# Kernel tuning notes

Hardware: AMD Instinct MI355X
Metric: run time of the kernel (lower is better)

## Reference

```python
import jax, jax.numpy as jnp
import numpy as np

B, S, H, DH = 2, 4096, 8, 64
D = H * DH


def setup_inputs() -> dict:
    key = jax.random.key(0)
    ks = jax.random.split(key, 6)
    std = 1.0 / np.sqrt(D)
    return {
        "x": jax.random.normal(ks[0], (B, S, D), dtype=jnp.float32),
        "Wq": jax.random.normal(ks[1], (D, D), dtype=jnp.float32) * std,
        "Wk": jax.random.normal(ks[2], (D, D), dtype=jnp.float32) * std,
        "Wv": jax.random.normal(ks[3], (D, D), dtype=jnp.float32) * std,
        "Wo": jax.random.normal(ks[4], (D, D), dtype=jnp.float32) * std,
        "bo": jnp.zeros((D,), dtype=jnp.float32),
    }


def reference(x, Wq, Wk, Wv, Wo, bo):
    scale = DH ** (-0.5)
    # torch Linear: y = x @ W.T
    q = x @ Wq.T  # [B,S,D]
    k = x @ Wk.T
    v = x @ Wv.T
    # split heads -> [B,H,S,Dh]
    q = q.reshape(B, S, H, DH).transpose(0, 2, 1, 3)
    k = k.reshape(B, S, H, DH).transpose(0, 2, 1, 3)
    v = v.reshape(B, S, H, DH).transpose(0, 2, 1, 3)
    score = jnp.einsum('bhqd,bhkd->bhqk', q, k) * scale  # [B,H,S,S]
    weights = jax.nn.softmax(score, axis=-1)
    attn = jnp.einsum('bhqk,bhkd->bhqd', weights, v)  # [B,H,S,Dh]
    h_ = attn.transpose(0, 2, 1, 3).reshape(B, S, D)
    return h_ @ Wo.T + bo
```

## Files before the change

### kernel.cpp

```cpp
#include <hip/hip_runtime.h>

#define LOG2E 1.44269504088896340736f

typedef unsigned short u16;
typedef __bf16 bf16x4_t __attribute__((ext_vector_type(4)));
typedef __bf16 bf16x8_t __attribute__((ext_vector_type(8)));
typedef float f32x4_t __attribute__((ext_vector_type(4)));

__device__ __forceinline__ f32x4_t mfma16(bf16x8_t a, bf16x8_t b, f32x4_t c) {
  return __builtin_amdgcn_mfma_f32_16x16x32_bf16(a, b, c, 0, 0, 0);
}

__device__ __forceinline__ void gl_lds16(const u16* g, u16* l) {
  __builtin_amdgcn_global_load_lds(
      (const __attribute__((address_space(1))) unsigned int*)g,
      (__attribute__((address_space(3))) unsigned int*)l, 16, 0, 0);
}

__global__ __launch_bounds__(256) void cast_kernel(
    const float* __restrict__ x, const float* __restrict__ Wq, const float* __restrict__ Wk,
    const float* __restrict__ Wv, const float* __restrict__ Wo,
    u16* __restrict__ Xb, u16* __restrict__ Wqb, u16* __restrict__ Wkb,
    u16* __restrict__ Wvb, u16* __restrict__ Wob) {
  const int bid = blockIdx.x;
  const float* src;
  u16* dst;
  float scale = 1.f;
  int rel;
  if (bid < 2048)      { src = x;  dst = Xb;  rel = bid; }
  else if (bid < 2176) { src = Wq; dst = Wqb; rel = bid - 2048; scale = 0.125f * LOG2E; }
  else if (bid < 2304) { src = Wk; dst = Wkb; rel = bid - 2176; }
  else if (bid < 2432) { src = Wv; dst = Wvb; rel = bid - 2304; }
  else                 { src = Wo; dst = Wob; rel = bid - 2432; }
  const int i = rel * 2048 + threadIdx.x * 8;
  f32x4_t a = *(const f32x4_t*)(src + i) * scale;
  f32x4_t b = *(const f32x4_t*)(src + i + 4) * scale;
  union { uint4 u; struct { bf16x4_t lo, hi; } s; } c;
  c.s.lo = __builtin_convertvector(a, bf16x4_t);
  c.s.hi = __builtin_convertvector(b, bf16x4_t);
  *(uint4*)(dst + i) = c.u;
}

template <int MODE>
__device__ __forceinline__ void gemm_core_bf16(const u16* __restrict__ A, const u16* __restrict__ Bt,
                                               void* __restrict__ Cout, const float* __restrict__ bo,
                                               int Mbase, int Nbase) {
  __shared__ __align__(16) u16 As[128][64];
  __shared__ __align__(16) u16 Bs[128][64];
  const int t = threadIdx.x;
  const int wave = t >> 6, lane = t & 63;
  const int r = lane & 15, qd = lane >> 4;
  const int wm = wave & 1, wn = wave >> 1;
  const int rr = lane >> 3;
  const int s8 = ((lane & 7) ^ (rr & 7)) * 8;

  f32x4_t acc[4][4];
#pragma unroll
  for (int i = 0; i < 4; i++)
#pragma unroll
    for (int j = 0; j < 4; j++) { f32x4_t z = {0.f, 0.f, 0.f, 0.f}; acc[i][j] = z; }

  const u16* pa = A  + (Mbase + wave * 32 + rr) * 512 + s8;
  const u16* pb = Bt + (Nbase + wave * 32 + rr) * 512 + s8;
  u16* la = &As[wave * 32][0];
  u16* lb = &Bs[wave * 32][0];

  for (int k0 = 0; k0 < 512; k0 += 64) {
#pragma unroll
    for (int j = 0; j < 4; j++) gl_lds16(pa + k0 + j * 8 * 512, la + j * 8 * 64);
#pragma unroll
    for (int j = 0; j < 4; j++) gl_lds16(pb + k0 + j * 8 * 512, lb + j * 8 * 64);
    __syncthreads();
#pragma unroll
    for (int h = 0; h < 2; h++) {
      bf16x8_t af[4], bfr[4];
#pragma unroll
      for (int i = 0; i < 4; i++)
        af[i]  = *(const bf16x8_t*)&As[wm * 64 + i * 16 + r][((h * 4 + qd) ^ (r & 7)) * 8];
#pragma unroll
      for (int j = 0; j < 4; j++)
        bfr[j] = *(const bf16x8_t*)&Bs[wn * 64 + j * 16 + r][((h * 4 + qd) ^ (r & 7)) * 8];
#pragma unroll
      for (int i = 0; i < 4; i++)
#pragma unroll
        for (int j = 0; j < 4; j++) acc[i][j] = mfma16(af[i], bfr[j], acc[i][j]);
    }
    __syncthreads();
  }

  float bv[4];
  if (MODE == 2) {
#pragma unroll
    for (int j = 0; j < 4; j++) bv[j] = bo[Nbase + wn * 64 + j * 16 + r];
  }
#pragma unroll
  for (int i = 0; i < 4; i++) {
#pragma unroll
    for (int reg = 0; reg < 4; reg++) {
      int gr = Mbase + wm * 64 + i * 16 + qd * 4 + reg;
#pragma unroll
      for (int j = 0; j < 4; j++) {
        int gc = Nbase + wn * 64 + j * 16 + r;
        float val = acc[i][j][reg];
        if (MODE == 1) {
          int bb = gc >> 12, ss = gc & 4095;
          ((__bf16*)Cout)[((long)(bb * 512 + gr)) * 4096 + ss] = (__bf16)val;
        } else if (MODE == 0) {
          ((__bf16*)Cout)[gr * 512 + gc] = (__bf16)val;
        } else {
          ((float*)Cout)[gr * 512 + gc] = val + bv[j];
        }
      }
    }
  }
}

__global__ __launch_bounds__(256) void gemm_qkv_kernel(
    const u16* __restrict__ Xb,
    const u16* __restrict__ Wqb, const u16* __restrict__ Wkb, const u16* __restrict__ Wvb,
    u16* __restrict__ Q, u16* __restrict__ K, u16* __restrict__ Vt) {
  if (blockIdx.z == 0)
    gemm_core_bf16<0>(Xb, Wqb, Q, nullptr, blockIdx.x * 128, blockIdx.y * 128);
  else if (blockIdx.z == 1)
    gemm_core_bf16<0>(Xb, Wkb, K, nullptr, blockIdx.x * 128, blockIdx.y * 128);
  else
    gemm_core_bf16<1>(Wvb, Xb, Vt, nullptr, blockIdx.y * 128, blockIdx.x * 128);
}

__global__ __launch_bounds__(256) void gemm_out_kernel(
    const u16* __restrict__ Aat, const u16* __restrict__ Wob,
    float* __restrict__ Out, const float* __restrict__ bo) {
  gemm_core_bf16<2>(Aat, Wob, Out, bo, blockIdx.x * 128, blockIdx.y * 128);
}

__global__ __launch_bounds__(256, 2) void attn_kernel(
    const u16* __restrict__ Q, const u16* __restrict__ K, const u16* __restrict__ Vt,
    u16* __restrict__ Oattn) {
  __shared__ __align__(16) u16 Ks[2][2][4096];
  __shared__ __align__(16) u16 Vs[2][2][4096];

  const int t = threadIdx.x;
  const int wave = t >> 6, lane = t & 63;
  const int r = lane & 15, qd = lane >> 4;
  const int g = wave & 1, kv = wave >> 1;
  const int bh = blockIdx.y;
  const int b = bh >> 3, h = bh & 7;
  const long bbase = (long)b * 4096 * 512;
  const int q0 = blockIdx.x * 128;

  const int sw = r & 7;
  const int ck0 = (qd ^ sw) * 8;
  const int ck1 = ((qd + 4) ^ sw) * 8;
  int vo0[2], vo1[2];
#pragma unroll
  for (int c = 0; c < 2; c++) {
    vo0[c] = ((c * 4 + (qd >> 1)) ^ sw) * 8 + 4 * (qd & 1);
    vo1[c] = ((c * 4 + 2 + (qd >> 1)) ^ sw) * 8 + 4 * (qd & 1);
  }

  bf16x8_t ones8;
#pragma unroll
  for (int j = 0; j < 8; j++) ones8[j] = (__bf16)1.0f;

  bf16x8_t qf[4][2];
#pragma unroll
  for (int qa = 0; qa < 4; qa++) {
    const u16* qp = Q + bbase + (long)(q0 + g * 64 + qa * 16 + r) * 512 + h * 64 + qd * 8;
    qf[qa][0] = *(const bf16x8_t*)(qp);
    qf[qa][1] = *(const bf16x8_t*)(qp + 32);
  }

  f32x4_t accO[4][4];
  f32x4_t accL[4];
#pragma unroll
  for (int qa = 0; qa < 4; qa++) {
    f32x4_t z = {0.f, 0.f, 0.f, 0.f};
    accL[qa] = z;
#pragma unroll
    for (int nt = 0; nt < 4; nt++) accO[qa][nt] = z;
  }

  const int rr = lane >> 3;
  const int cc = (lane & 7) ^ rr;
  const u16* kgb = K + bbase + (long)(kv * 2048 + g * 32 + rr) * 512 + h * 64 + cc * 8;
  const u16* vgb = Vt + ((long)(b * 512 + h * 64 + g * 32 + rr)) * 4096 + kv * 2048 + cc * 8;

#pragma unroll
  for (int i = 0; i < 4; i++) gl_lds16(kgb + (long)i * 8 * 512, &Ks[kv][0][g * 2048] + i * 512);
#pragma unroll
  for (int i = 0; i < 4; i++) gl_lds16(vgb + i * 8 * 4096, &Vs[kv][0][g * 2048] + i * 512);

  for (int it = 0; it < 32; it++) {
    const int buf = it & 1;
    __syncthreads();

    if (it < 31) {
      const int nb = (it + 1) & 1;
      const long ko = (long)(it + 1) * 64;
#pragma unroll
      for (int i = 0; i < 4; i++)
        gl_lds16(kgb + (ko + i * 8) * 512, &Ks[kv][nb][g * 2048] + i * 512);
#pragma unroll
      for (int i = 0; i < 4; i++)
        gl_lds16(vgb + ko + (long)i * 8 * 4096, &Vs[kv][nb][g * 2048] + i * 512);
    }

    bf16x8_t kf[4][2];
#pragma unroll
    for (int nt = 0; nt < 4; nt++) {
      const u16* kb = &Ks[kv][buf][(nt * 16 + r) * 64];
      kf[nt][0] = *(const bf16x8_t*)(kb + ck0);
      kf[nt][1] = *(const bf16x8_t*)(kb + ck1);
    }

    f32x4_t St[4][4];
    __builtin_amdgcn_s_setprio(1);
#pragma unroll
    for (int qa = 0; qa < 4; qa++)
#pragma unroll
      for (int nt = 0; nt < 4; nt++) {
        f32x4_t z = {0.f, 0.f, 0.f, 0.f};
        z = mfma16(kf[nt][0], qf[qa][0], z);
        z = mfma16(kf[nt][1], qf[qa][1], z);
        St[qa][nt] = z;
      }
    __builtin_amdgcn_s_setprio(0);

    bf16x8_t pf[4][2];
#pragma unroll
    for (int qa = 0; qa < 4; qa++)
#pragma unroll
      for (int c = 0; c < 2; c++) {
        f32x4_t e0, e1;
#pragma unroll
        for (int j = 0; j < 4; j++) {
          e0[j] = __builtin_amdgcn_exp2f(St[qa][2 * c][j]);
          e1[j] = __builtin_amdgcn_exp2f(St[qa][2 * c + 1][j]);
        }
        bf16x4_t b0 = __builtin_convertvector(e0, bf16x4_t);
        bf16x4_t b1 = __builtin_convertvector(e1, bf16x4_t);
        bf16x8_t p8;
#pragma unroll
        for (int j = 0; j < 4; j++) { p8[j] = b0[j]; p8[4 + j] = b1[j]; }
        pf[qa][c] = p8;
      }

#pragma unroll
    for (int qa = 0; qa < 4; qa++)
#pragma unroll
      for (int c = 0; c < 2; c++)
        accL[qa] = mfma16(ones8, pf[qa][c], accL[qa]);

#pragma unroll
    for (int c = 0; c < 2; c++) {
      bf16x8_t va[4];
#pragma unroll
      for (int dm = 0; dm < 4; dm++) {
        const u16* vb = &Vs[kv][buf][(dm * 16 + r) * 64];
        union { uint4 u; bf16x8_t v; } cat;
        *(uint2*)&cat.u.x = *(const uint2*)(vb + vo0[c]);
        *(uint2*)&cat.u.z = *(const uint2*)(vb + vo1[c]);
        va[dm] = cat.v;
      }
      __builtin_amdgcn_s_setprio(1);
#pragma unroll
      for (int qa = 0; qa < 4; qa++)
#pragma unroll
        for (int dm = 0; dm < 4; dm++)
          accO[qa][dm] = mfma16(va[dm], pf[qa][c], accO[qa][dm]);
      __builtin_amdgcn_s_setprio(0);
    }
  }

  __syncthreads();
  float* Sc  = (float*)&Ks[0][0][0];
  float* Lsc = (float*)&Vs[0][0][0];
  if (kv == 1) {
#pragma unroll
    for (int qa = 0; qa < 4; qa++) {
#pragma unroll
      for (int dm = 0; dm < 4; dm++)
        *(f32x4_t*)&Sc[g * 4096 + ((qa * 4 + dm) * 64 + lane) * 4] = accO[qa][dm];
      Lsc[g * 256 + qa * 64 + lane] = accL[qa][0];
    }
  }
  __syncthreads();
  if (kv == 0) {
#pragma unroll
    for (int qa = 0; qa < 4; qa++) {
      float L = accL[qa][0] + Lsc[g * 256 + qa * 64 + lane];
      float inv = 1.f / L;
      int gq = q0 + g * 64 + qa * 16 + r;
#pragma unroll
      for (int dm = 0; dm < 4; dm++) {
        f32x4_t o = *(const f32x4_t*)&Sc[g * 4096 + ((qa * 4 + dm) * 64 + lane) * 4];
        o += accO[qa][dm];
        bf16x4_t ob;
#pragma unroll
        for (int reg = 0; reg < 4; reg++) ob[reg] = (__bf16)(o[reg] * inv);
        *(uint2*)&Oattn[bbase + (long)gq * 512 + h * 64 + dm * 16 + qd * 4] = *(uint2*)&ob;
      }
    }
  }
}

extern "C" void kernel_launch(void* const* d_in, const int* in_sizes, int n_in,
                              void* d_out, int out_size, void* d_ws, size_t ws_size,
                              hipStream_t stream) {
  const float* x  = (const float*)d_in[0];
  const float* Wq = (const float*)d_in[1];
  const float* Wk = (const float*)d_in[2];
  const float* Wv = (const float*)d_in[3];
  const float* Wo = (const float*)d_in[4];
  const float* bo = (const float*)d_in[5];
  float* out = (float*)d_out;

  u16* ws  = (u16*)d_ws;
  u16* Qb  = ws;
  u16* Kb  = Qb  + 4194304;
  u16* Vtg = Kb  + 4194304;
  u16* Ab  = Vtg + 4194304;
  u16* Xb  = Ab;
  u16* Wqb = Ab  + 4194304;
  u16* Wkb = Wqb + 262144;
  u16* Wvb = Wkb + 262144;
  u16* Wob = Wvb + 262144;

  cast_kernel<<<2560, 256, 0, stream>>>(x, Wq, Wk, Wv, Wo, Xb, Wqb, Wkb, Wvb, Wob);

  dim3 g1(64, 4, 3);
  gemm_qkv_kernel<<<g1, 256, 0, stream>>>(Xb, Wqb, Wkb, Wvb, Qb, Kb, Vtg);

  dim3 g2(32, 16);
  attn_kernel<<<g2, 256, 0, stream>>>(Qb, Kb, Vtg, Ab);

  dim3 g3(64, 4);
  gemm_out_kernel<<<g3, 256, 0, stream>>>(Ab, Wob, out, bo);
}
```

Baseline: 186.7 us.

## Fuse QKV projections into one kernel with shared X tile and LDS-staged stores

```diff
diff --git a/kernel.cpp b/kernel.cpp
--- a/kernel.cpp
+++ b/kernel.cpp
@@ -41,96 +41,171 @@
   *(uint4*)(dst + i) = c.u;
 }
 
-template <int MODE>
-__device__ __forceinline__ void gemm_core_bf16(const u16* __restrict__ A, const u16* __restrict__ Bt,
-                                               void* __restrict__ Cout, const float* __restrict__ bo,
-                                               int Mbase, int Nbase) {
-  __shared__ __align__(16) u16 As[128][64];
-  __shared__ __align__(16) u16 Bs[128][64];
+__global__ __launch_bounds__(512) void gemm_qkv_fused(
+    const u16* __restrict__ Xb,
+    const u16* __restrict__ Wqb, const u16* __restrict__ Wkb, const u16* __restrict__ Wvb,
+    u16* __restrict__ Q, u16* __restrict__ K, u16* __restrict__ Vt) {
+  __shared__ __align__(16) u16 SM[28672];
+  u16 (*As)[64] = (u16(*)[64])SM;
+  u16 (*Bq)[64] = (u16(*)[64])(SM + 4096);
+  u16 (*Bk)[64] = (u16(*)[64])(SM + 12288);
+  u16 (*Bv)[64] = (u16(*)[64])(SM + 20480);
   const int t = threadIdx.x;
   const int wave = t >> 6, lane = t & 63;
   const int r = lane & 15, qd = lane >> 4;
-  const int wm = wave & 1, wn = wave >> 1;
+  const int wn = wave;
   const int rr = lane >> 3;
   const int s8 = ((lane & 7) ^ (rr & 7)) * 8;
-
-  f32x4_t acc[4][4];
+  const int Mbase = blockIdx.x * 64, Nbase = blockIdx.y * 128;
+
+  f32x4_t acc[3][4];
+#pragma unroll
+  for (int w = 0; w < 3; w++)
+#pragma unroll
+    for (int i = 0; i < 4; i++) { f32x4_t z = {0.f, 0.f, 0.f, 0.f}; acc[w][i] = z; }
+
+  const u16* pa = Xb  + (Mbase + wave * 8 + rr) * 512 + s8;
+  const u16* pq = Wqb + (Nbase + wave * 16 + rr) * 512 + s8;
+  const u16* pk = Wkb + (Nbase + wave * 16 + rr) * 512 + s8;
+  const u16* pv = Wvb + (Nbase + wave * 16 + rr) * 512 + s8;
+  u16* la = &As[wave * 8][0];
+  u16* lq = &Bq[wave * 16][0];
+  u16* lk = &Bk[wave * 16][0];
+  u16* lv = &Bv[wave * 16][0];
+
+  for (int k0 = 0; k0 < 512; k0 += 64) {
+    gl_lds16(pa + k0, la);
+#pragma unroll
+    for (int p = 0; p < 2; p++) {
+      gl_lds16(pq + k0 + p * 8 * 512, lq + p * 512);
+      gl_lds16(pk + k0 + p * 8 * 512, lk + p * 512);
+      gl_lds16(pv + k0 + p * 8 * 512, lv + p * 512);
+    }
+    __syncthreads();
+#pragma unroll
+    for (int h = 0; h < 2; h++) {
+      const int cs = ((h * 4 + qd) ^ (r & 7)) * 8;
+      bf16x8_t af[4];
+#pragma unroll
+      for (int i = 0; i < 4; i++) af[i] = *(const bf16x8_t*)&As[i * 16 + r][cs];
+      bf16x8_t fq = *(const bf16x8_t*)&Bq[wn * 16 + r][cs];
+      bf16x8_t fk = *(const bf16x8_t*)&Bk[wn * 16 + r][cs];
+      bf16x8_t fv = *(const bf16x8_t*)&Bv[wn * 16 + r][cs];
+#pragma unroll
+      for (int i = 0; i < 4; i++) {
+        acc[0][i] = mfma16(af[i], fq, acc[0][i]);
+        acc[1][i] = mfma16(af[i], fk, acc[1][i]);
+        acc[2][i] = mfma16(af[i], fv, acc[2][i]);
+      }
+    }
+    __syncthreads();
+  }
+
+#pragma unroll
+  for (int w = 0; w < 2; w++) {
+    __syncthreads();
+    u16* dst = (w == 0) ? Q : K;
+#pragma unroll
+    for (int i = 0; i < 4; i++)
+#pragma unroll
+      for (int reg = 0; reg < 4; reg++) {
+        int row = i * 16 + qd * 4 + reg;
+        int col = wn * 16 + r;
+        __bf16 bvv = (__bf16)acc[w][i][reg];
+        SM[row * 128 + (col ^ (((row >> 2) & 7) << 3))] = *(u16*)&bvv;
+      }
+    __syncthreads();
+#pragma unroll
+    for (int p = 0; p < 2; p++) {
+      int row = p * 32 + (t >> 4);
+      int col = (t & 15) * 8;
+      uint4 v = *(const uint4*)&SM[row * 128 + (col ^ (((row >> 2) & 7) << 3))];
+      *(uint4*)&dst[(Mbase + row) * 512 + Nbase + col] = v;
+    }
+  }
+  __syncthreads();
 #pragma unroll
   for (int i = 0; i < 4; i++)
 #pragma unroll
-    for (int j = 0; j < 4; j++) { f32x4_t z = {0.f, 0.f, 0.f, 0.f}; acc[i][j] = z; }
-
-  const u16* pa = A  + (Mbase + wave * 32 + rr) * 512 + s8;
-  const u16* pb = Bt + (Nbase + wave * 32 + rr) * 512 + s8;
-  u16* la = &As[wave * 32][0];
-  u16* lb = &Bs[wave * 32][0];
-
-  for (int k0 = 0; k0 < 512; k0 += 64) {
-#pragma unroll
-    for (int j = 0; j < 4; j++) gl_lds16(pa + k0 + j * 8 * 512, la + j * 8 * 64);
-#pragma unroll
-    for (int j = 0; j < 4; j++) gl_lds16(pb + k0 + j * 8 * 512, lb + j * 8 * 64);
-    __syncthreads();
-#pragma unroll
-    for (int h = 0; h < 2; h++) {
-      bf16x8_t af[4], bfr[4];
-#pragma unroll
-      for (int i = 0; i < 4; i++)
-        af[i]  = *(const bf16x8_t*)&As[wm * 64 + i * 16 + r][((h * 4 + qd) ^ (r & 7)) * 8];
-#pragma unroll
-      for (int j = 0; j < 4; j++)
-        bfr[j] = *(const bf16x8_t*)&Bs[wn * 64 + j * 16 + r][((h * 4 + qd) ^ (r & 7)) * 8];
-#pragma unroll
-      for (int i = 0; i < 4; i++)
-#pragma unroll
-        for (int j = 0; j < 4; j++) acc[i][j] = mfma16(af[i], bfr[j], acc[i][j]);
-    }
-    __syncthreads();
-  }
-
-  float bv[4];
-  if (MODE == 2) {
-#pragma unroll
-    for (int j = 0; j < 4; j++) bv[j] = bo[Nbase + wn * 64 + j * 16 + r];
-  }
-#pragma unroll
-  for (int i = 0; i < 4; i++) {
-#pragma unroll
     for (int reg = 0; reg < 4; reg++) {
-      int gr = Mbase + wm * 64 + i * 16 + qd * 4 + reg;
-#pragma unroll
-      for (int j = 0; j < 4; j++) {
-        int gc = Nbase + wn * 64 + j * 16 + r;
-        float val = acc[i][j][reg];
-        if (MODE == 1) {
-          int bb = gc >> 12, ss = gc & 4095;
-          ((__bf16*)Cout)[((long)(bb * 512 + gr)) * 4096 + ss] = (__bf16)val;
-        } else if (MODE == 0) {
-          ((__bf16*)Cout)[gr * 512 + gc] = (__bf16)val;
-        } else {
-          ((float*)Cout)[gr * 512 + gc] = val + bv[j];
-        }
-      }
-    }
-  }
-}
-
-__global__ __launch_bounds__(256) void gemm_qkv_kernel(
-    const u16* __restrict__ Xb,
-    const u16* __restrict__ Wqb, const u16* __restrict__ Wkb, const u16* __restrict__ Wvb,
-    u16* __restrict__ Q, u16* __restrict__ K, u16* __restrict__ Vt) {
-  if (blockIdx.z == 0)
-    gemm_core_bf16<0>(Xb, Wqb, Q, nullptr, blockIdx.x * 128, blockIdx.y * 128);
-  else if (blockIdx.z == 1)
-    gemm_core_bf16<0>(Xb, Wkb, K, nullptr, blockIdx.x * 128, blockIdx.y * 128);
-  else
-    gemm_core_bf16<1>(Wvb, Xb, Vt, nullptr, blockIdx.y * 128, blockIdx.x * 128);
-}
-
-__global__ __launch_bounds__(256) void gemm_out_kernel(
+      int srow = i * 16 + qd * 4 + reg;
+      int dcol = wn * 16 + r;
+      __bf16 bvv = (__bf16)acc[2][i][reg];
+      SM[dcol * 64 + (srow ^ (((dcol >> 2) & 7) << 3))] = *(u16*)&bvv;
+    }
+  __syncthreads();
+  {
+    const int bb = Mbase >> 12;
+    const int smod = Mbase & 4095;
+#pragma unroll
+    for (int p = 0; p < 2; p++) {
+      int d = p * 64 + (t >> 3);
+      int scol = (t & 7) * 8;
+      uint4 v = *(const uint4*)&SM[d * 64 + (scol ^ (((d >> 2) & 7) << 3))];
+      *(uint4*)&Vt[((long)(bb * 512 + Nbase + d)) * 4096 + smod + scol] = v;
+    }
+  }
+}
+
+__global__ __launch_bounds__(512) void gemm_out_kernel(
     const u16* __restrict__ Aat, const u16* __restrict__ Wob,
     float* __restrict__ Out, const float* __restrict__ bo) {
-  gemm_core_bf16<2>(Aat, Wob, Out, bo, blockIdx.x * 128, blockIdx.y * 128);
+  __shared__ __align__(16) u16 SM[16384];
+  u16 (*As)[64] = (u16(*)[64])SM;
+  u16 (*Bs)[64] = (u16(*)[64])(SM + 4096);
+  const int t = threadIdx.x;
+  const int wave = t >> 6, lane = t & 63;
+  const int r = lane & 15, qd = lane >> 4;
+  const int wn = wave;
+  const int rr = lane >> 3;
+  const int s8 = ((lane & 7) ^ (rr & 7)) * 8;
+  const int Mbase = blockIdx.x * 64, Nbase = blockIdx.y * 128;
+
+  f32x4_t acc[4];
+#pragma unroll
+  for (int i = 0; i < 4; i++) { f32x4_t z = {0.f, 0.f, 0.f, 0.f}; acc[i] = z; }
+
+  const u16* pa = Aat + (Mbase + wave * 8 + rr) * 512 + s8;
+  const u16* pb = Wob + (Nbase + wave * 16 + rr) * 512 + s8;
+  u16* la = &As[wave * 8][0];
+  u16* lb = &Bs[wave * 16][0];
+
+  for (int k0 = 0; k0 < 512; k0 += 64) {
+    gl_lds16(pa + k0, la);
+#pragma unroll
+    for (int p = 0; p < 2; p++) gl_lds16(pb + k0 + p * 8 * 512, lb + p * 512);
+    __syncthreads();
+#pragma unroll
+    for (int h = 0; h < 2; h++) {
+      const int cs = ((h * 4 + qd) ^ (r & 7)) * 8;
+      bf16x8_t af[4];
+#pragma unroll
+      for (int i = 0; i < 4; i++) af[i] = *(const bf16x8_t*)&As[i * 16 + r][cs];
+      bf16x8_t bfr = *(const bf16x8_t*)&Bs[wn * 16 + r][cs];
+#pragma unroll
+      for (int i = 0; i < 4; i++) acc[i] = mfma16(af[i], bfr, acc[i]);
+    }
+    __syncthreads();
+  }
+
+  float* stf = (float*)SM;
+  float bv = bo[Nbase + wn * 16 + r];
+#pragma unroll
+  for (int i = 0; i < 4; i++)
+#pragma unroll
+    for (int reg = 0; reg < 4; reg++) {
+      int row = i * 16 + qd * 4 + reg;
+      int col = wn * 16 + r;
+      stf[row * 128 + (col ^ (((row >> 2) & 7) << 2))] = acc[i][reg] + bv;
+    }
+  __syncthreads();
+#pragma unroll
+  for (int p = 0; p < 4; p++) {
+    int row = p * 16 + (t >> 5);
+    int col4 = (t & 31) * 4;
+    f32x4_t v = *(const f32x4_t*)&stf[row * 128 + (col4 ^ (((row >> 2) & 7) << 2))];
+    *(f32x4_t*)&Out[(Mbase + row) * 512 + Nbase + col4] = v;
+  }
 }
 
 __global__ __launch_bounds__(256, 2) void attn_kernel(
@@ -328,12 +403,12 @@
 
   cast_kernel<<<2560, 256, 0, stream>>>(x, Wq, Wk, Wv, Wo, Xb, Wqb, Wkb, Wvb, Wob);
 
-  dim3 g1(64, 4, 3);
-  gemm_qkv_kernel<<<g1, 256, 0, stream>>>(Xb, Wqb, Wkb, Wvb, Qb, Kb, Vtg);
+  dim3 g1(128, 4);
+  gemm_qkv_fused<<<g1, 512, 0, stream>>>(Xb, Wqb, Wkb, Wvb, Qb, Kb, Vtg);
 
   dim3 g2(32, 16);
   attn_kernel<<<g2, 256, 0, stream>>>(Qb, Kb, Vtg, Ab);
 
-  dim3 g3(64, 4);
-  gemm_out_kernel<<<g3, 256, 0, stream>>>(Ab, Wob, out, bo);
-}
+  dim3 g3(128, 4);
+  gemm_out_kernel<<<g3, 512, 0, stream>>>(Ab, Wob, out, bo);
+}
```

New measurement: 177.2 us, median of 2. 5.1% less time.
